# Optimization experiments

Hardware: AMD Instinct MI355X
Metric: run time of the kernel (lower is better)

The kernel has to match this reference:

```python
import jax, jax.numpy as jnp
import numpy as np

NUM = 4
EPS = 1e-8


def setup_inputs() -> dict:
    key = jax.random.key(0)
    ks = jax.random.split(key, 8)
    B, N, D = 64, 1024, 512
    x = jax.random.normal(ks[0], (B, N, D), dtype=jnp.float32)
    # marginal priors: valid probability distributions (log is taken inside)
    p0 = jax.nn.softmax(jax.random.normal(ks[1], (B, 1, D), dtype=jnp.float32), axis=2)
    q0 = jax.nn.softmax(jax.random.normal(ks[2], (B, N, 1), dtype=jnp.float32), axis=1)
    # strictly positive regularization weights / ADMM step sizes
    a1 = jax.random.uniform(ks[3], (NUM,), dtype=jnp.float32, minval=0.1, maxval=1.1)
    a2 = jax.random.uniform(ks[4], (NUM,), dtype=jnp.float32, minval=0.1, maxval=1.1)
    a3 = jax.random.uniform(ks[5], (NUM,), dtype=jnp.float32, minval=0.1, maxval=1.1)
    rho = jax.random.uniform(ks[6], (NUM,), dtype=jnp.float32, minval=0.1, maxval=1.1)
    mask = jnp.ones((B, N, 1), dtype=jnp.float32)
    return {"x": x, "p0": p0, "q0": q0, "a1": a1, "a2": a2, "a3": a3,
            "rho": rho, "mask": mask}


def _lse(y, axis):
    return jax.scipy.special.logsumexp(y, axis=axis, keepdims=True)


def _masked_log_colsum(y, mask):
    # stable log(sum_n exp(y)*mask) over axis 1, masking as in the torch code
    ymin = jnp.min(y, axis=1, keepdims=True)
    ymax = jnp.max(ymin - mask * ymin + y, axis=1, keepdims=True)
    lse = jnp.log(jnp.sum(jnp.exp((y - ymax) * mask) * mask, axis=1, keepdims=True))
    return lse, ymax


def uot_badmm(x, p0, q0, a1, a2, a3, rho, mask, num=NUM, eps=EPS):
    log_p0 = jnp.log(p0)                      # (B,1,D)
    log_q0 = jnp.log(q0 + eps) * mask         # (B,N,1)
    log_t = (log_q0 + log_p0) * mask          # (B,N,D)
    log_s = (log_q0 + log_p0) * mask
    log_mu = jnp.log(p0)
    log_eta = jnp.log(q0 + eps) * mask
    z = jnp.zeros_like(log_t)
    z1 = jnp.zeros_like(p0)
    z2 = jnp.zeros_like(q0)
    for k in range(num):
        n = min(k, a1.shape[0] - 1)
        rn = rho[n]
        # t-update
        y = (x - z) / rn + log_s
        log_t = mask * (log_eta - _lse(y, 2)) + y
        # s-update
        y = (z + rn * log_t) / (a1[n] + rn)
        lse, ymax = _masked_log_colsum(y, mask)
        log_s = mask * (log_mu - lse - ymax) + y
        t = jnp.exp(log_t) * mask
        s = jnp.exp(log_s) * mask
        z = z + rn * (t - s)
        # mu-update
        y = (rn * log_mu + a2[n] * log_p0 - z1) / (rn + a2[n])
        log_mu = y - _lse(y, 2)
        # eta-update
        y = (rn * log_eta + a3[n] * log_q0 - z2) / (rn + a3[n])
        lse, ymax = _masked_log_colsum(y, mask)
        log_eta = (y - lse - ymax) * mask
        # dual updates
        z1 = z1 + rn * (jnp.exp(log_mu) - jnp.sum(s, axis=1, keepdims=True))
        z2 = z2 + rn * (jnp.exp(log_eta) * mask - jnp.sum(t, axis=2, keepdims=True)) * mask
    return jnp.exp(log_t) * mask


def reference(x, p0, q0, a1, a2, a3, rho, mask):
    return uot_badmm(x, p0, q0, a1, a2, a3, rho, mask, num=NUM, eps=EPS)
```

## Files before the change

### kernel.cpp

```cpp
#include <hip/hip_runtime.h>
#include <math.h>

#define BB 64
#define NN 1024
#define DD 512
#define SEG 64
#define ROWS_PER_BLOCK 16
#define ROWS_PER_WAVE 4
#define WAVES 4
#define EPSQ 1e-8f
#define L2E 1.44269504088896340736f

typedef float f32x4 __attribute__((ext_vector_type(4)));

#if __has_builtin(__builtin_amdgcn_exp2f)
__device__ __forceinline__ float ex2(float x) { return __builtin_amdgcn_exp2f(x); }
#else
__device__ __forceinline__ float ex2(float x) { return exp2f(x); }
#endif
#if __has_builtin(__builtin_amdgcn_logf)
__device__ __forceinline__ float lg2(float x) { return __builtin_amdgcn_logf(x); }
#else
__device__ __forceinline__ float lg2(float x) { return log2f(x); }
#endif

__device__ __forceinline__ float wmax(float v) {
#pragma unroll
    for (int o = 32; o; o >>= 1) v = fmaxf(v, __shfl_xor(v, o));
    return v;
}
__device__ __forceinline__ float wsum(float v) {
#pragma unroll
    for (int o = 32; o; o >>= 1) v += __shfl_xor(v, o);
    return v;
}
template <int NW>
__device__ __forceinline__ float block_max(float v, float* lds) {
    v = wmax(v);
    __syncthreads();
    if ((threadIdx.x & 63) == 0) lds[threadIdx.x >> 6] = v;
    __syncthreads();
    float r = lds[0];
#pragma unroll
    for (int i = 1; i < NW; i++) r = fmaxf(r, lds[i]);
    return r;
}
template <int NW>
__device__ __forceinline__ float block_sum(float v, float* lds) {
    v = wsum(v);
    __syncthreads();
    if ((threadIdx.x & 63) == 0) lds[threadIdx.x >> 6] = v;
    __syncthreads();
    float r = 0.f;
#pragma unroll
    for (int i = 0; i < NW; i++) r += lds[i];
    return r;
}

__device__ __forceinline__ void load8(float* r, const float* p) {
    float4 a = *reinterpret_cast<const float4*>(p);
    float4 b = *reinterpret_cast<const float4*>(p + 4);
    r[0] = a.x; r[1] = a.y; r[2] = a.z; r[3] = a.w;
    r[4] = b.x; r[5] = b.y; r[6] = b.z; r[7] = b.w;
}
__device__ __forceinline__ void store8_nt(float* p, const float* r) {
    f32x4 a, b;
    a.x = r[0]; a.y = r[1]; a.z = r[2]; a.w = r[3];
    b.x = r[4]; b.y = r[5]; b.z = r[6]; b.w = r[7];
    __builtin_nontemporal_store(a, reinterpret_cast<f32x4*>(p));
    __builtin_nontemporal_store(b, reinterpret_cast<f32x4*>(p) + 1);
}

__global__ __launch_bounds__(256, 4) void k1_kernel(
    const float* __restrict__ x, const float* __restrict__ p0,
    const float* __restrict__ q0, const float* __restrict__ a1,
    const float* __restrict__ a2, const float* __restrict__ a3,
    const float* __restrict__ rho, float* __restrict__ lmu_seq,
    float* __restrict__ leta_seq, float* __restrict__ lp_tab,
    float* __restrict__ crow, float* __restrict__ psum) {
    __shared__ float sms[WAVES][DD];
    __shared__ float s_red[8];
    const int tid = threadIdx.x;

    if (blockIdx.x < BB) {
        const int b = blockIdx.x;
        const float lpA = lg2(p0[b * DD + tid]);
        const float lpB = lg2(p0[b * DD + tid + 256]);
        lp_tab[b * DD + tid] = lpA;
        lp_tab[b * DD + tid + 256] = lpB;
        float lqv[4], lev[4], z2v[4];
#pragma unroll
        for (int u = 0; u < 4; u++) {
            lqv[u] = lg2(q0[b * NN + tid + 256 * u] + EPSQ);
            lev[u] = lqv[u];
            z2v[u] = 0.f;
            leta_seq[b * NN + tid + 256 * u] = lqv[u];
        }
        float lmuA = lpA, lmuB = lpB, z1A = 0.f, z1B = 0.f;
        lmu_seq[b * DD + tid] = lmuA;
        lmu_seq[b * DD + tid + 256] = lmuB;
        for (int k = 0; k < 3; k++) {
            const float r = rho[k], A2 = a2[k], A3 = a3[k];
            const float rL = r * L2E;
            float yA = (r * lmuA + A2 * lpA - z1A) / (r + A2);
            float yB = (r * lmuB + A2 * lpB - z1B) / (r + A2);
            float m = block_max<4>(fmaxf(yA, yB), s_red);
            float S = block_sum<4>(ex2(yA - m) + ex2(yB - m), s_red);
            float lse = m + lg2(S);
            float lmuAn = yA - lse, lmuBn = yB - lse;
            z1A += rL * (ex2(lmuAn) - ex2(lmuA));
            z1B += rL * (ex2(lmuBn) - ex2(lmuB));
            lmuA = lmuAn;
            lmuB = lmuBn;
            if (k < 2) {
                lmu_seq[(size_t)(k + 1) * (BB * DD) + b * DD + tid] = lmuA;
                lmu_seq[(size_t)(k + 1) * (BB * DD) + b * DD + tid + 256] = lmuB;
            }
            float yv[4];
            float ml = -INFINITY;
#pragma unroll
            for (int u = 0; u < 4; u++) {
                yv[u] = (r * lev[u] + A3 * lqv[u] - z2v[u]) / (r + A3);
                ml = fmaxf(ml, yv[u]);
            }
            m = block_max<4>(ml, s_red);
            float se = 0.f;
#pragma unroll
            for (int u = 0; u < 4; u++) se += ex2(yv[u] - m);
            S = block_sum<4>(se, s_red);
            lse = m + lg2(S);
#pragma unroll
            for (int u = 0; u < 4; u++) {
                float ln = yv[u] - lse;
                z2v[u] += rL * (ex2(ln) - ex2(lev[u]));
                lev[u] = ln;
                leta_seq[(size_t)(k + 1) * (BB * NN) + b * NN + tid + 256 * u] = ln;
            }
        }
        return;
    }

    const int blk = blockIdx.x - BB;
    const int b = blk >> 6, seg = blk & 63;
    const int w = tid >> 6, l = tid & 63;
    const int d0 = l * 8;
    const float r0 = rho[0];
    const float inv_r0 = 1.f / r0;
    const float inv_ar0 = 1.f / (a1[0] + r0);

    float lp[8];
    {
        float tmp[8];
        load8(tmp, p0 + b * DD + d0);
#pragma unroll
        for (int j = 0; j < 8; j++) lp[j] = lg2(tmp[j]);
    }

    float ss[8];
#pragma unroll
    for (int j = 0; j < 8; j++) ss[j] = 0.f;

    const int row0 = seg * ROWS_PER_BLOCK + w * ROWS_PER_WAVE;
#pragma unroll
    for (int i = 0; i < ROWS_PER_WAVE; i++) {
        const int n = row0 + i;
        const size_t base = ((size_t)b * NN + n) * DD + d0;
        const float lq = lg2(q0[b * NN + n] + EPSQ);
        float xv[8];
        load8(xv, x + base);
        float yb[8];
        float se = 0.f;
#pragma unroll
        for (int j = 0; j < 8; j++) {
            float xs = xv[j] * L2E;
            yb[j] = fmaf(xs, inv_r0, lq + lp[j]);
            se += ex2(yb[j]);
        }
        float lse = lg2(wsum(se));
        const float c = lq - lse;
        if (l == 0) crow[b * NN + n] = c;
#pragma unroll
        for (int j = 0; j < 8; j++) {
            float lt = c + yb[j];
            ss[j] += ex2((r0 * lt) * inv_ar0);
        }
    }
#pragma unroll
    for (int j = 0; j < 8; j += 4)
        *reinterpret_cast<float4*>(&sms[w][d0 + j]) =
            make_float4(ss[j], ss[j + 1], ss[j + 2], ss[j + 3]);
    __syncthreads();
    for (int d = tid; d < DD; d += 256) {
        float S = sms[0][d] + sms[1][d] + sms[2][d] + sms[3][d];
        psum[((size_t)b * SEG + seg) * DD + d] = S;
    }
}

__global__ __launch_bounds__(256) void colfin_kernel(
    const float* __restrict__ psum, const float* __restrict__ lmu_seq,
    float* __restrict__ cc_tab, int k) {
    const int idx = blockIdx.x * 256 + threadIdx.x;
    const int b = idx >> 9, d = idx & (DD - 1);
    float S = 0.f;
    for (int s = 0; s < SEG; s++)
        S += psum[((size_t)b * SEG + s) * DD + d];
    cc_tab[(size_t)k * (BB * DD) + idx] =
        lmu_seq[(size_t)k * (BB * DD) + idx] - lg2(S);
}

template <int P, bool LAST>
__global__ __launch_bounds__(256, 4) void f_kernel(
    const float* __restrict__ x, float* __restrict__ out,
    const float* __restrict__ lp_tab, const float* __restrict__ leta_seq,
    float* __restrict__ crow, const float* __restrict__ cc_tab,
    float* __restrict__ psum, const float* __restrict__ a1,
    const float* __restrict__ rho) {
    __shared__ float sms[WAVES][DD];
    const int b = blockIdx.x >> 6, seg = blockIdx.x & 63;
    const int w = threadIdx.x >> 6, l = threadIdx.x & 63;
    const int d0 = l * 8;

    float rv[P + 1], invr[P + 1], rLv[P + 1], invar[P + 1];
#pragma unroll
    for (int i = 0; i <= P; i++) {
        rv[i] = rho[i];
        invr[i] = 1.f / rv[i];
        rLv[i] = rv[i] * L2E;
        invar[i] = 1.f / (a1[i] + rv[i]);
    }

    float lp[8];
    load8(lp, lp_tab + b * DD + d0);
    float ccv[P][8];
#pragma unroll
    for (int i = 0; i < P; i++)
        load8(ccv[i], cc_tab + (size_t)i * (BB * DD) + b * DD + d0);

    const float* lrowq = leta_seq + b * NN;
    const float* lrowP = leta_seq + (size_t)P * (BB * NN) + b * NN;

    float ss[8];
#pragma unroll
    for (int j = 0; j < 8; j++) ss[j] = 0.f;

    const int row0 = seg * ROWS_PER_BLOCK + w * ROWS_PER_WAVE;
#pragma unroll
    for (int i0 = 0; i0 < ROWS_PER_WAVE; i0++) {
        const int n = row0 + i0;
        const size_t base = ((size_t)b * NN + n) * DD + d0;
        float xv[8];
        load8(xv, x + base);
        const float lq = lrowq[n];
        float cr[P];
#pragma unroll
        for (int i = 0; i < P; i++)
            cr[i] = crow[(size_t)i * (BB * NN) + b * NN + n];
        const float letaP = lrowP[n];
        float yb[8], znj[8];
        float se = 0.f;
#pragma unroll
        for (int j = 0; j < 8; j++) {
            float xs = xv[j] * L2E;
            float y = fmaf(xs, invr[0], lq + lp[j]);
            float lt = cr[0] + y;
            float zn = 0.f;
#pragma unroll
            for (int i = 1; i <= P; i++) {
                float y2v = (zn + rv[i - 1] * lt) * invar[i - 1];
                float ls = ccv[i - 1][j] + y2v;
                zn = zn + rLv[i - 1] * (ex2(lt) - ex2(ls));
                y = fmaf(xs - zn, invr[i], ls);
                if (i < P) lt = cr[i] + y;
            }
            yb[j] = y;
            znj[j] = zn;
            se += ex2(y);
        }
        float lse = lg2(wsum(se));
        const float c = letaP - lse;
        if (LAST) {
            float o[8];
#pragma unroll
            for (int j = 0; j < 8; j++) o[j] = ex2(c + yb[j]);
            store8_nt(out + base, o);
        } else {
            if (l == 0) crow[(size_t)P * (BB * NN) + b * NN + n] = c;
#pragma unroll
            for (int j = 0; j < 8; j++) {
                float lt = c + yb[j];
                float y2P = (znj[j] + rv[P] * lt) * invar[P];
                ss[j] += ex2(y2P);
            }
        }
    }
    if (!LAST) {
#pragma unroll
        for (int j = 0; j < 8; j += 4)
            *reinterpret_cast<float4*>(&sms[w][d0 + j]) =
                make_float4(ss[j], ss[j + 1], ss[j + 2], ss[j + 3]);
        __syncthreads();
        for (int d = threadIdx.x; d < DD; d += 256) {
            float S = sms[0][d] + sms[1][d] + sms[2][d] + sms[3][d];
            psum[((size_t)b * SEG + seg) * DD + d] = S;
        }
    }
}

extern "C" void kernel_launch(void* const* d_in, const int* in_sizes, int n_in,
                              void* d_out, int out_size, void* d_ws,
                              size_t ws_size, hipStream_t stream) {
    (void)in_sizes; (void)n_in; (void)out_size; (void)ws_size;
    const float* x = (const float*)d_in[0];
    const float* p0 = (const float*)d_in[1];
    const float* q0 = (const float*)d_in[2];
    const float* a1 = (const float*)d_in[3];
    const float* a2 = (const float*)d_in[4];
    const float* a3 = (const float*)d_in[5];
    const float* rho = (const float*)d_in[6];
    float* out = (float*)d_out;

    char* w = (char*)d_ws;
    float* lmu_seq = (float*)w;    w += (size_t)3 * BB * DD * 4;
    float* leta_seq = (float*)w;   w += (size_t)4 * BB * NN * 4;
    float* psum = (float*)w;       w += (size_t)BB * SEG * DD * 4;
    float* cc_tab = (float*)w;     w += (size_t)3 * BB * DD * 4;
    float* crow = (float*)w;       w += (size_t)3 * BB * NN * 4;
    float* lp_tab = (float*)w;

    const int blocks = BB * SEG;
    const int cfin_blocks = (BB * DD) / 256;

    k1_kernel<<<BB + blocks, 256, 0, stream>>>(x, p0, q0, a1, a2, a3, rho,
                                               lmu_seq, leta_seq, lp_tab, crow,
                                               psum);

    colfin_kernel<<<cfin_blocks, 256, 0, stream>>>(psum, lmu_seq, cc_tab, 0);
    f_kernel<1, false><<<blocks, 256, 0, stream>>>(
        x, out, lp_tab, leta_seq, crow, cc_tab, psum, a1, rho);

    colfin_kernel<<<cfin_blocks, 256, 0, stream>>>(psum, lmu_seq, cc_tab, 1);
    f_kernel<2, false><<<blocks, 256, 0, stream>>>(
        x, out, lp_tab, leta_seq, crow, cc_tab, psum, a1, rho);

    colfin_kernel<<<cfin_blocks, 256, 0, stream>>>(psum, lmu_seq, cc_tab, 2);
    f_kernel<3, true><<<blocks, 256, 0, stream>>>(
        x, out, lp_tab, leta_seq, crow, cc_tab, psum, a1, rho);
}
```

Measured before the change: 153.2 us.

## Fuse column-sum finalization into f_kernel prologue with ping-pong partial sums

Removes the three separate colfin launches. Each f_kernel block now reduces the 64 partial column sums for its batch itself and computes the column correction into shared memory. Block seg 0 writes that correction to cc_tab for later passes, and psum uses double buffering to avoid read/write races across launches. Each of the 64 blocks per batch redundantly reads 64x512 partial sums (128KB per block) in exchange for fewer launches. The last pass also factors exp(c+y) into exp(c)*exp(y), reusing the exponentials already computed for the row sum.

```diff
diff --git a/kernel.cpp b/kernel.cpp
--- a/kernel.cpp
+++ b/kernel.cpp
@@ -196,29 +196,30 @@
     }
 }
 
-__global__ __launch_bounds__(256) void colfin_kernel(
-    const float* __restrict__ psum, const float* __restrict__ lmu_seq,
-    float* __restrict__ cc_tab, int k) {
-    const int idx = blockIdx.x * 256 + threadIdx.x;
-    const int b = idx >> 9, d = idx & (DD - 1);
-    float S = 0.f;
-    for (int s = 0; s < SEG; s++)
-        S += psum[((size_t)b * SEG + s) * DD + d];
-    cc_tab[(size_t)k * (BB * DD) + idx] =
-        lmu_seq[(size_t)k * (BB * DD) + idx] - lg2(S);
-}
-
 template <int P, bool LAST>
 __global__ __launch_bounds__(256, 4) void f_kernel(
     const float* __restrict__ x, float* __restrict__ out,
     const float* __restrict__ lp_tab, const float* __restrict__ leta_seq,
-    float* __restrict__ crow, const float* __restrict__ cc_tab,
-    float* __restrict__ psum, const float* __restrict__ a1,
+    float* __restrict__ crow, float* __restrict__ cc_tab,
+    const float* __restrict__ lmu_seq, const float* __restrict__ psum_in,
+    float* __restrict__ psum_out, const float* __restrict__ a1,
     const float* __restrict__ rho) {
     __shared__ float sms[WAVES][DD];
+    __shared__ float s_cc[DD];
     const int b = blockIdx.x >> 6, seg = blockIdx.x & 63;
     const int w = threadIdx.x >> 6, l = threadIdx.x & 63;
     const int d0 = l * 8;
+
+    for (int d = threadIdx.x; d < DD; d += 256) {
+        float S = 0.f;
+        for (int s = 0; s < SEG; s++)
+            S += psum_in[((size_t)b * SEG + s) * DD + d];
+        float cc = lmu_seq[(size_t)(P - 1) * (BB * DD) + b * DD + d] - lg2(S);
+        s_cc[d] = cc;
+        if (!LAST && seg == 0)
+            cc_tab[(size_t)(P - 1) * (BB * DD) + b * DD + d] = cc;
+    }
+    __syncthreads();
 
     float rv[P + 1], invr[P + 1], rLv[P + 1], invar[P + 1];
 #pragma unroll
@@ -233,8 +234,9 @@
     load8(lp, lp_tab + b * DD + d0);
     float ccv[P][8];
 #pragma unroll
-    for (int i = 0; i < P; i++)
+    for (int i = 0; i + 1 < P; i++)
         load8(ccv[i], cc_tab + (size_t)i * (BB * DD) + b * DD + d0);
+    load8(ccv[P - 1], &s_cc[d0]);
 
     const float* lrowq = leta_seq + b * NN;
     const float* lrowP = leta_seq + (size_t)P * (BB * NN) + b * NN;
@@ -272,16 +274,22 @@
                 y = fmaf(xs - zn, invr[i], ls);
                 if (i < P) lt = cr[i] + y;
             }
-            yb[j] = y;
+            if (LAST) {
+                yb[j] = ex2(y);
+                se += yb[j];
+            } else {
+                yb[j] = y;
+                se += ex2(y);
+            }
             znj[j] = zn;
-            se += ex2(y);
         }
         float lse = lg2(wsum(se));
         const float c = letaP - lse;
         if (LAST) {
+            const float ec = ex2(c);
             float o[8];
 #pragma unroll
-            for (int j = 0; j < 8; j++) o[j] = ex2(c + yb[j]);
+            for (int j = 0; j < 8; j++) o[j] = ec * yb[j];
             store8_nt(out + base, o);
         } else {
             if (l == 0) crow[(size_t)P * (BB * NN) + b * NN + n] = c;
@@ -301,7 +309,7 @@
         __syncthreads();
         for (int d = threadIdx.x; d < DD; d += 256) {
             float S = sms[0][d] + sms[1][d] + sms[2][d] + sms[3][d];
-            psum[((size_t)b * SEG + seg) * DD + d] = S;
+            psum_out[((size_t)b * SEG + seg) * DD + d] = S;
         }
     }
 }
@@ -322,27 +330,21 @@
     char* w = (char*)d_ws;
     float* lmu_seq = (float*)w;    w += (size_t)3 * BB * DD * 4;
     float* leta_seq = (float*)w;   w += (size_t)4 * BB * NN * 4;
-    float* psum = (float*)w;       w += (size_t)BB * SEG * DD * 4;
-    float* cc_tab = (float*)w;     w += (size_t)3 * BB * DD * 4;
+    float* psumA = (float*)w;      w += (size_t)BB * SEG * DD * 4;
+    float* psumB = (float*)w;      w += (size_t)BB * SEG * DD * 4;
+    float* cc_tab = (float*)w;     w += (size_t)2 * BB * DD * 4;
     float* crow = (float*)w;       w += (size_t)3 * BB * NN * 4;
     float* lp_tab = (float*)w;
 
     const int blocks = BB * SEG;
-    const int cfin_blocks = (BB * DD) / 256;
 
     k1_kernel<<<BB + blocks, 256, 0, stream>>>(x, p0, q0, a1, a2, a3, rho,
                                                lmu_seq, leta_seq, lp_tab, crow,
-                                               psum);
-
-    colfin_kernel<<<cfin_blocks, 256, 0, stream>>>(psum, lmu_seq, cc_tab, 0);
+                                               psumA);
     f_kernel<1, false><<<blocks, 256, 0, stream>>>(
-        x, out, lp_tab, leta_seq, crow, cc_tab, psum, a1, rho);
-
-    colfin_kernel<<<cfin_blocks, 256, 0, stream>>>(psum, lmu_seq, cc_tab, 1);
+        x, out, lp_tab, leta_seq, crow, cc_tab, lmu_seq, psumA, psumB, a1, rho);
     f_kernel<2, false><<<blocks, 256, 0, stream>>>(
-        x, out, lp_tab, leta_seq, crow, cc_tab, psum, a1, rho);
-
-    colfin_kernel<<<cfin_blocks, 256, 0, stream>>>(psum, lmu_seq, cc_tab, 2);
+        x, out, lp_tab, leta_seq, crow, cc_tab, lmu_seq, psumB, psumA, a1, rho);
     f_kernel<3, true><<<blocks, 256, 0, stream>>>(
-        x, out, lp_tab, leta_seq, crow, cc_tab, psum, a1, rho);
-}
+        x, out, lp_tab, leta_seq, crow, cc_tab, lmu_seq, psumA, psumB, a1, rho);
+}
```

After: 197.7 us. 1.29x slower.
